# Kernel tuning notes

Hardware: AMD Instinct MI355X
Metric: run time of the kernel (lower is better)

Reference implementation:

```python
import jax, jax.numpy as jnp
import numpy as np

# Segment geometry (from init_kwargs): modes ['u','uv','v'] -> out_v = alpha * x_u @ W_uv
U = 128
V = 128
IN_OFF = [0, 128, 256, 384]
W_OFF = [k * U * V for k in range(8)]          # [0,16384,...,114688]
OUT_OFF = [0, 128, 256, 384]
IN_STRIDE = 512
OUT_STRIDE = 512
W_STRIDE = 8 * U * V                           # 131072
# (in_seg, w_seg, out_seg, coefficient)
PATHS = [(0, 0, 0, 1.0), (1, 1, 1, 1.0), (2, 2, 2, 1.0), (3, 3, 3, 1.0),
         (0, 4, 1, 0.5), (1, 5, 2, 0.5), (2, 6, 3, 0.5), (3, 7, 0, 0.5)]
B = 32768
E = 4  # num_embeddings (experts)


def setup_inputs() -> dict:
    key = jax.random.key(0)
    k1, k2, k3 = jax.random.split(key, 3)
    tensor_in = jax.random.normal(k1, (B, IN_STRIDE), dtype=jnp.float32)
    tensor_w = jax.random.normal(k2, (E, W_STRIDE), dtype=jnp.float32)
    tensor_w_id = jax.random.randint(k3, (B,), 0, E, dtype=jnp.int32)
    return {"tensor_in": tensor_in, "tensor_w": tensor_w, "tensor_w_id": tensor_w_id}


def _batch_linear(tensor_in, tensor_w, tensor_w_id):
    """Segmented path-indexed grouped linear (cuEquivariance BatchLinear fwd).

    tensor_in: [B, IN_STRIDE]; tensor_w: [E, W_STRIDE]; tensor_w_id: [B] int in [0,E).
    For each path (i, j, k, alpha):
        out[b, OUT_OFF[k]:+V] += alpha * x[b, IN_OFF[i]:+U] @ W[w_id[b], seg j].reshape(U, V)
    """
    nb = tensor_in.shape[0]
    ne = tensor_w.shape[0]
    onehot = jax.nn.one_hot(tensor_w_id, ne, dtype=tensor_in.dtype)  # [B, E]
    out = jnp.zeros((nb, OUT_STRIDE), dtype=tensor_in.dtype)
    for (i, j, k, a) in PATHS:
        x = tensor_in[:, IN_OFF[i]:IN_OFF[i] + U]                    # [B, U]
        w_seg = tensor_w[:, W_OFF[j]:W_OFF[j] + U * V].reshape(ne, U, V)
        # masked per-expert dense GEMMs (small fixed expert count)
        y = jnp.zeros((nb, V), dtype=tensor_in.dtype)
        for e in range(ne):
            y = y + onehot[:, e:e + 1] * (x @ w_seg[e])              # [B, V]
        out = out.at[:, OUT_OFF[k]:OUT_OFF[k] + V].add(a * y)
    return out


def reference(tensor_in, tensor_w, tensor_w_id):
    return _batch_linear(tensor_in, tensor_w, tensor_w_id)
```

## Files before the change

### kernel.cpp

```cpp
#include <hip/hip_runtime.h>
#include <stdint.h>

#define U 128
#define V 128
#define IN_STRIDE 512
#define OUT_STRIDE 512
#define W_STRIDE (8 * U * V)
#define NB 32768
#define NE 4

#define WS_WSHUF 0
#define WS_CNT   1048576
#define WS_SORT  1048640

typedef __bf16 bf16x8 __attribute__((ext_vector_type(8)));
typedef float f32x16 __attribute__((ext_vector_type(16)));
typedef unsigned int u32x4 __attribute__((ext_vector_type(4)));
typedef unsigned int u32x2 __attribute__((ext_vector_type(2)));

static __device__ __forceinline__ unsigned short f2bf(float f) {
    unsigned int u = __builtin_bit_cast(unsigned int, f);
    u += 0x7FFFu + ((u >> 16) & 1u);
    return (unsigned short)(u >> 16);
}

__global__ void prep_kernel(const float* __restrict__ w, unsigned short* __restrict__ wshuf,
                            unsigned int* __restrict__ cnt) {
    if (blockIdx.x == 0 && threadIdx.x < NE) cnt[threadIdx.x] = 0u;
    int t = blockIdx.x * 256 + threadIdx.x;
    int lane = t & 63;
    int kt = (t >> 6) & 7;
    int nt = (t >> 9) & 3;
    int s  = (t >> 11) & 7;
    int e  = (t >> 14) & 3;
    int kbase = kt * 16 + ((lane >> 5) << 3);
    int n = nt * 32 + (lane & 31);
    const float* src = w + (size_t)e * W_STRIDE + (size_t)s * (U * V) + n;
    float sc = (s >= 4) ? 0.5f : 1.0f;
    __attribute__((aligned(16))) unsigned short o[8];
#pragma unroll
    for (int j = 0; j < 8; j++) o[j] = f2bf(src[(size_t)(kbase + j) * V] * sc);
    *(u32x4*)(wshuf + (size_t)t * 8) = *(const u32x4*)o;
}

__global__ void scatter_kernel(const int* __restrict__ wid, unsigned int* __restrict__ cnt,
                               int* __restrict__ sorted) {
    __shared__ unsigned int lcnt[NE];
    __shared__ unsigned int lbase[NE];
    int t = threadIdx.x;
    if (t < NE) lcnt[t] = 0u;
    __syncthreads();
    int i = blockIdx.x * 256 + t;
    int e = wid[i];
    unsigned int lpos = atomicAdd(&lcnt[e], 1u);
    __syncthreads();
    if (t < NE) lbase[t] = atomicAdd(&cnt[t], lcnt[t]);
    __syncthreads();
    sorted[e * NB + (int)(lbase[e] + lpos)] = i;
}

__global__ __launch_bounds__(512, 4) void gemm_kernel(
        const float* __restrict__ x, const unsigned short* __restrict__ wshuf,
        const unsigned int* __restrict__ cnt, const int* __restrict__ sorted,
        float* __restrict__ out) {
    const int rowbase = blockIdx.x * 64;
    __shared__ unsigned short lds[64 * 512];
    __shared__ int rowid[64];

    const unsigned int p1 = cnt[0];
    const unsigned int p2 = p1 + cnt[1];
    const unsigned int p3 = p2 + cnt[2];

    const int t = threadIdx.x;

    {
        int r = t >> 3;
        int g = t & 7;
        unsigned int l = (unsigned int)(rowbase + r);
        int e = (l >= p1) + (l >= p2) + (l >= p3);
        unsigned int pe = (e == 0) ? 0u : (e == 1) ? p1 : (e == 2) ? p2 : p3;
        int row = sorted[e * NB + (int)(l - pe)];
        if (g == 0) rowid[r] = row;
        const float* xr = x + (size_t)row * IN_STRIDE;
        unsigned short* Lrow = lds + r * 512;
        int rs = r & 7;
#pragma unroll
        for (int i = 0; i < 16; i++) {
            int c = g * 4 + i * 32;
            float4 v = *(const float4*)(xr + c);
            __attribute__((aligned(8))) unsigned short h[4];
            h[0] = f2bf(v.x); h[1] = f2bf(v.y); h[2] = f2bf(v.z); h[3] = f2bf(v.w);
            int off = ((((c >> 3) ^ rs)) << 3) + (c & 7);
            *(u32x2*)(Lrow + off) = *(const u32x2*)h;
        }
    }

    const int w = t >> 6, lane = t & 63;
    const int kout = w >> 1, nhalf = w & 1;
    const int m0 = lane & 31;
    const int khalf3 = (lane >> 5);
    const int rowswz = m0 & 7;

    const unsigned int l0 = (unsigned int)(rowbase + m0);
    const unsigned int l1 = l0 + 32u;
    const int e0 = (l0 >= p1) + (l0 >= p2) + (l0 >= p3);
    const int e1 = (l1 >= p1) + (l1 >= p2) + (l1 >= p3);
    const unsigned int lh = (unsigned int)rowbase, lt = (unsigned int)(rowbase + 63);
    const int ehead = (lh >= p1) + (lh >= p2) + (lh >= p3);
    const int etail = (lt >= p1) + (lt >= p2) + (lt >= p3);

    __syncthreads();

    f32x16 acc00 = {}, acc01 = {}, acc10 = {}, acc11 = {};

    const int xbs1 = (kout + 3) & 3;
    int xbs[2] = {kout, xbs1};
    int sgs[2] = {kout, xbs1 + 4};

    const unsigned short* Lr0 = lds + m0 * 512;
    const unsigned short* Lr1 = lds + (m0 + 32) * 512;

    if (ehead == etail) {
        const int eu = ehead;
#pragma unroll
        for (int c = 0; c < 2; c++) {
            int colbase3 = xbs[c] * 16;
            const unsigned short* wseg =
                wshuf + ((size_t)((eu * 8 + sgs[c]) * 4 + nhalf * 2) * 8) * 512 + (size_t)lane * 8;
#pragma unroll
            for (int kt = 0; kt < 8; kt++) {
                int kabs3 = colbase3 + kt * 2 + khalf3;
                int packoff = ((kabs3 ^ rowswz) << 3);
                bf16x8 a0 = __builtin_bit_cast(bf16x8, *(const u32x4*)(Lr0 + packoff));
                bf16x8 a1 = __builtin_bit_cast(bf16x8, *(const u32x4*)(Lr1 + packoff));
                bf16x8 b0 = __builtin_bit_cast(bf16x8, *(const u32x4*)(wseg + (size_t)kt * 512));
                bf16x8 b1 = __builtin_bit_cast(bf16x8, *(const u32x4*)(wseg + (size_t)(8 + kt) * 512));
                acc00 = __builtin_amdgcn_mfma_f32_32x32x16_bf16(a0, b0, acc00, 0, 0, 0);
                acc01 = __builtin_amdgcn_mfma_f32_32x32x16_bf16(a0, b1, acc01, 0, 0, 0);
                acc10 = __builtin_amdgcn_mfma_f32_32x32x16_bf16(a1, b0, acc10, 0, 0, 0);
                acc11 = __builtin_amdgcn_mfma_f32_32x32x16_bf16(a1, b1, acc11, 0, 0, 0);
            }
        }
    } else {
        unsigned int msk0[4], msk1[4];
#pragma unroll
        for (int e = 0; e < 4; e++) {
            msk0[e] = (e0 == e) ? 0xFFFFFFFFu : 0u;
            msk1[e] = (e1 == e) ? 0xFFFFFFFFu : 0u;
        }
#pragma unroll
        for (int c = 0; c < 2; c++) {
            int colbase3 = xbs[c] * 16;
#pragma unroll
            for (int kt = 0; kt < 8; kt++) {
                int kabs3 = colbase3 + kt * 2 + khalf3;
                int packoff = ((kabs3 ^ rowswz) << 3);
                u32x4 a0u = *(const u32x4*)(Lr0 + packoff);
                u32x4 a1u = *(const u32x4*)(Lr1 + packoff);
#pragma unroll
                for (int e = 0; e < 4; e++) {
                    const unsigned short* wseg =
                        wshuf + ((size_t)((e * 8 + sgs[c]) * 4 + nhalf * 2) * 8) * 512;
                    bf16x8 b0 = __builtin_bit_cast(bf16x8, *(const u32x4*)(wseg + (size_t)kt * 512 + lane * 8));
                    bf16x8 b1 = __builtin_bit_cast(bf16x8, *(const u32x4*)(wseg + (size_t)(8 + kt) * 512 + lane * 8));
                    u32x4 mm0 = {msk0[e], msk0[e], msk0[e], msk0[e]};
                    u32x4 mm1 = {msk1[e], msk1[e], msk1[e], msk1[e]};
                    bf16x8 a0m = __builtin_bit_cast(bf16x8, a0u & mm0);
                    bf16x8 a1m = __builtin_bit_cast(bf16x8, a1u & mm1);
                    acc00 = __builtin_amdgcn_mfma_f32_32x32x16_bf16(a0m, b0, acc00, 0, 0, 0);
                    acc01 = __builtin_amdgcn_mfma_f32_32x32x16_bf16(a0m, b1, acc01, 0, 0, 0);
                    acc10 = __builtin_amdgcn_mfma_f32_32x32x16_bf16(a1m, b0, acc10, 0, 0, 0);
                    acc11 = __builtin_amdgcn_mfma_f32_32x32x16_bf16(a1m, b1, acc11, 0, 0, 0);
                }
            }
        }
    }

    const int colb = kout * 128 + nhalf * 64 + m0;
    const int rh = (lane >> 5) << 2;
#pragma unroll
    for (int q = 0; q < 4; q++) {
#pragma unroll
        for (int d = 0; d < 4; d++) {
            int reg = q * 4 + d;
            int rl = d + 8 * q + rh;
            float* o0 = out + (size_t)rowid[rl] * OUT_STRIDE + colb;
            float* o1 = out + (size_t)rowid[rl + 32] * OUT_STRIDE + colb;
            o0[0]  = acc00[reg];
            o0[32] = acc01[reg];
            o1[0]  = acc10[reg];
            o1[32] = acc11[reg];
        }
    }
}

extern "C" void kernel_launch(void* const* d_in, const int* in_sizes, int n_in,
                              void* d_out, int out_size, void* d_ws, size_t ws_size,
                              hipStream_t stream) {
    const float* x = (const float*)d_in[0];
    const float* w = (const float*)d_in[1];
    const int* wid = (const int*)d_in[2];
    float* out = (float*)d_out;

    unsigned short* wshuf = (unsigned short*)((char*)d_ws + WS_WSHUF);
    unsigned int* cnt = (unsigned int*)((char*)d_ws + WS_CNT);
    int* sorted = (int*)((char*)d_ws + WS_SORT);

    prep_kernel<<<256, 256, 0, stream>>>(w, wshuf, cnt);
    scatter_kernel<<<128, 256, 0, stream>>>(wid, cnt, sorted);
    gemm_kernel<<<512, 512, 0, stream>>>(x, wshuf, cnt, sorted, out);
}
```

Before: 134.9 us.

## Drop LDS staging; load activations directly into MFMA registers with 32-row tiles

The GEMM kernel no longer stages bf16-converted activation rows in shared memory. Each wave now loads its A fragment straight from global fp32, converts it in registers, and covers all four 32-column N tiles of one output block, with 32 rows per workgroup of 256 threads. This removes the LDS footprint, the barrier and the staging pass, and should raise occupancy. In exchange each x element is loaded and converted by two waves instead of once, weight fragments are reused across fewer rows, and the output row ids are recomputed from the sorted index rather than read from shared memory.

```diff
diff --git a/kernel.cpp b/kernel.cpp
--- a/kernel.cpp
+++ b/kernel.cpp
@@ -16,7 +16,6 @@
 typedef __bf16 bf16x8 __attribute__((ext_vector_type(8)));
 typedef float f32x16 __attribute__((ext_vector_type(16)));
 typedef unsigned int u32x4 __attribute__((ext_vector_type(4)));
-typedef unsigned int u32x2 __attribute__((ext_vector_type(2)));
 
 static __device__ __forceinline__ unsigned short f2bf(float f) {
     unsigned int u = __builtin_bit_cast(unsigned int, f);
@@ -59,137 +58,111 @@
     sorted[e * NB + (int)(lbase[e] + lpos)] = i;
 }
 
-__global__ __launch_bounds__(512, 4) void gemm_kernel(
+__global__ __launch_bounds__(256, 4) void gemm_kernel(
         const float* __restrict__ x, const unsigned short* __restrict__ wshuf,
         const unsigned int* __restrict__ cnt, const int* __restrict__ sorted,
         float* __restrict__ out) {
-    const int rowbase = blockIdx.x * 64;
-    __shared__ unsigned short lds[64 * 512];
-    __shared__ int rowid[64];
-
+    const int rowbase = blockIdx.x * 32;
     const unsigned int p1 = cnt[0];
     const unsigned int p2 = p1 + cnt[1];
     const unsigned int p3 = p2 + cnt[2];
 
     const int t = threadIdx.x;
-
-    {
-        int r = t >> 3;
-        int g = t & 7;
-        unsigned int l = (unsigned int)(rowbase + r);
-        int e = (l >= p1) + (l >= p2) + (l >= p3);
-        unsigned int pe = (e == 0) ? 0u : (e == 1) ? p1 : (e == 2) ? p2 : p3;
-        int row = sorted[e * NB + (int)(l - pe)];
-        if (g == 0) rowid[r] = row;
-        const float* xr = x + (size_t)row * IN_STRIDE;
-        unsigned short* Lrow = lds + r * 512;
-        int rs = r & 7;
-#pragma unroll
-        for (int i = 0; i < 16; i++) {
-            int c = g * 4 + i * 32;
-            float4 v = *(const float4*)(xr + c);
-            __attribute__((aligned(8))) unsigned short h[4];
-            h[0] = f2bf(v.x); h[1] = f2bf(v.y); h[2] = f2bf(v.z); h[3] = f2bf(v.w);
-            int off = ((((c >> 3) ^ rs)) << 3) + (c & 7);
-            *(u32x2*)(Lrow + off) = *(const u32x2*)h;
-        }
-    }
-
-    const int w = t >> 6, lane = t & 63;
-    const int kout = w >> 1, nhalf = w & 1;
+    const int kout = t >> 6;
+    const int lane = t & 63;
     const int m0 = lane & 31;
-    const int khalf3 = (lane >> 5);
-    const int rowswz = m0 & 7;
+    const int khalf = lane >> 5;
 
     const unsigned int l0 = (unsigned int)(rowbase + m0);
-    const unsigned int l1 = l0 + 32u;
     const int e0 = (l0 >= p1) + (l0 >= p2) + (l0 >= p3);
-    const int e1 = (l1 >= p1) + (l1 >= p2) + (l1 >= p3);
-    const unsigned int lh = (unsigned int)rowbase, lt = (unsigned int)(rowbase + 63);
+    const unsigned int pe0 = (e0 == 0) ? 0u : (e0 == 1) ? p1 : (e0 == 2) ? p2 : p3;
+    const int arow = sorted[e0 * NB + (int)(l0 - pe0)];
+    const float* xr = x + (size_t)arow * IN_STRIDE + khalf * 8;
+
+    const unsigned int lh = (unsigned int)rowbase, lt = (unsigned int)(rowbase + 31);
     const int ehead = (lh >= p1) + (lh >= p2) + (lh >= p3);
     const int etail = (lt >= p1) + (lt >= p2) + (lt >= p3);
-
-    __syncthreads();
-
-    f32x16 acc00 = {}, acc01 = {}, acc10 = {}, acc11 = {};
 
     const int xbs1 = (kout + 3) & 3;
     int xbs[2] = {kout, xbs1};
     int sgs[2] = {kout, xbs1 + 4};
 
-    const unsigned short* Lr0 = lds + m0 * 512;
-    const unsigned short* Lr1 = lds + (m0 + 32) * 512;
+    f32x16 acc[4] = {};
 
     if (ehead == etail) {
         const int eu = ehead;
 #pragma unroll
         for (int c = 0; c < 2; c++) {
-            int colbase3 = xbs[c] * 16;
-            const unsigned short* wseg =
-                wshuf + ((size_t)((eu * 8 + sgs[c]) * 4 + nhalf * 2) * 8) * 512 + (size_t)lane * 8;
+            const unsigned short* wb =
+                wshuf + (size_t)((eu * 8 + sgs[c]) * 4) * 4096 + (size_t)lane * 8;
+            const float* xc = xr + xbs[c] * 128;
 #pragma unroll
             for (int kt = 0; kt < 8; kt++) {
-                int kabs3 = colbase3 + kt * 2 + khalf3;
-                int packoff = ((kabs3 ^ rowswz) << 3);
-                bf16x8 a0 = __builtin_bit_cast(bf16x8, *(const u32x4*)(Lr0 + packoff));
-                bf16x8 a1 = __builtin_bit_cast(bf16x8, *(const u32x4*)(Lr1 + packoff));
-                bf16x8 b0 = __builtin_bit_cast(bf16x8, *(const u32x4*)(wseg + (size_t)kt * 512));
-                bf16x8 b1 = __builtin_bit_cast(bf16x8, *(const u32x4*)(wseg + (size_t)(8 + kt) * 512));
-                acc00 = __builtin_amdgcn_mfma_f32_32x32x16_bf16(a0, b0, acc00, 0, 0, 0);
-                acc01 = __builtin_amdgcn_mfma_f32_32x32x16_bf16(a0, b1, acc01, 0, 0, 0);
-                acc10 = __builtin_amdgcn_mfma_f32_32x32x16_bf16(a1, b0, acc10, 0, 0, 0);
-                acc11 = __builtin_amdgcn_mfma_f32_32x32x16_bf16(a1, b1, acc11, 0, 0, 0);
+                float4 va = *(const float4*)(xc + kt * 16);
+                float4 vb = *(const float4*)(xc + kt * 16 + 4);
+                bf16x8 a;
+                a[0] = (__bf16)va.x; a[1] = (__bf16)va.y;
+                a[2] = (__bf16)va.z; a[3] = (__bf16)va.w;
+                a[4] = (__bf16)vb.x; a[5] = (__bf16)vb.y;
+                a[6] = (__bf16)vb.z; a[7] = (__bf16)vb.w;
+#pragma unroll
+                for (int nt = 0; nt < 4; nt++) {
+                    bf16x8 b = __builtin_bit_cast(bf16x8,
+                        *(const u32x4*)(wb + (size_t)(nt * 8 + kt) * 512));
+                    acc[nt] = __builtin_amdgcn_mfma_f32_32x32x16_bf16(a, b, acc[nt], 0, 0, 0);
+                }
             }
         }
     } else {
-        unsigned int msk0[4], msk1[4];
+        unsigned int msk[4];
 #pragma unroll
-        for (int e = 0; e < 4; e++) {
-            msk0[e] = (e0 == e) ? 0xFFFFFFFFu : 0u;
-            msk1[e] = (e1 == e) ? 0xFFFFFFFFu : 0u;
-        }
+        for (int e = 0; e < 4; e++) msk[e] = (e0 == e) ? 0xFFFFFFFFu : 0u;
 #pragma unroll
         for (int c = 0; c < 2; c++) {
-            int colbase3 = xbs[c] * 16;
+            const float* xc = xr + xbs[c] * 128;
 #pragma unroll
             for (int kt = 0; kt < 8; kt++) {
-                int kabs3 = colbase3 + kt * 2 + khalf3;
-                int packoff = ((kabs3 ^ rowswz) << 3);
-                u32x4 a0u = *(const u32x4*)(Lr0 + packoff);
-                u32x4 a1u = *(const u32x4*)(Lr1 + packoff);
+                float4 va = *(const float4*)(xc + kt * 16);
+                float4 vb = *(const float4*)(xc + kt * 16 + 4);
+                __attribute__((aligned(16))) unsigned short au[8];
+                au[0] = f2bf(va.x); au[1] = f2bf(va.y);
+                au[2] = f2bf(va.z); au[3] = f2bf(va.w);
+                au[4] = f2bf(vb.x); au[5] = f2bf(vb.y);
+                au[6] = f2bf(vb.z); au[7] = f2bf(vb.w);
+                u32x4 araw = *(const u32x4*)au;
 #pragma unroll
                 for (int e = 0; e < 4; e++) {
-                    const unsigned short* wseg =
-                        wshuf + ((size_t)((e * 8 + sgs[c]) * 4 + nhalf * 2) * 8) * 512;
-                    bf16x8 b0 = __builtin_bit_cast(bf16x8, *(const u32x4*)(wseg + (size_t)kt * 512 + lane * 8));
-                    bf16x8 b1 = __builtin_bit_cast(bf16x8, *(const u32x4*)(wseg + (size_t)(8 + kt) * 512 + lane * 8));
-                    u32x4 mm0 = {msk0[e], msk0[e], msk0[e], msk0[e]};
-                    u32x4 mm1 = {msk1[e], msk1[e], msk1[e], msk1[e]};
-                    bf16x8 a0m = __builtin_bit_cast(bf16x8, a0u & mm0);
-                    bf16x8 a1m = __builtin_bit_cast(bf16x8, a1u & mm1);
-                    acc00 = __builtin_amdgcn_mfma_f32_32x32x16_bf16(a0m, b0, acc00, 0, 0, 0);
-                    acc01 = __builtin_amdgcn_mfma_f32_32x32x16_bf16(a0m, b1, acc01, 0, 0, 0);
-                    acc10 = __builtin_amdgcn_mfma_f32_32x32x16_bf16(a1m, b0, acc10, 0, 0, 0);
-                    acc11 = __builtin_amdgcn_mfma_f32_32x32x16_bf16(a1m, b1, acc11, 0, 0, 0);
+                    u32x4 mm = {msk[e], msk[e], msk[e], msk[e]};
+                    bf16x8 am = __builtin_bit_cast(bf16x8, araw & mm);
+                    const unsigned short* wb =
+                        wshuf + (size_t)((e * 8 + sgs[c]) * 4) * 4096 + (size_t)lane * 8;
+#pragma unroll
+                    for (int nt = 0; nt < 4; nt++) {
+                        bf16x8 b = __builtin_bit_cast(bf16x8,
+                            *(const u32x4*)(wb + (size_t)(nt * 8 + kt) * 512));
+                        acc[nt] = __builtin_amdgcn_mfma_f32_32x32x16_bf16(am, b, acc[nt], 0, 0, 0);
+                    }
                 }
             }
         }
     }
 
-    const int colb = kout * 128 + nhalf * 64 + m0;
-    const int rh = (lane >> 5) << 2;
+    const int colb = kout * 128 + m0;
+    const int rh = khalf << 2;
 #pragma unroll
     for (int q = 0; q < 4; q++) {
 #pragma unroll
         for (int d = 0; d < 4; d++) {
             int reg = q * 4 + d;
-            int rl = d + 8 * q + rh;
-            float* o0 = out + (size_t)rowid[rl] * OUT_STRIDE + colb;
-            float* o1 = out + (size_t)rowid[rl + 32] * OUT_STRIDE + colb;
-            o0[0]  = acc00[reg];
-            o0[32] = acc01[reg];
-            o1[0]  = acc10[reg];
-            o1[32] = acc11[reg];
+            unsigned int ls = (unsigned int)(rowbase + d + 8 * q + rh);
+            int es = (ls >= p1) + (ls >= p2) + (ls >= p3);
+            unsigned int pes = (es == 0) ? 0u : (es == 1) ? p1 : (es == 2) ? p2 : p3;
+            int orow = sorted[es * NB + (int)(ls - pes)];
+            float* o = out + (size_t)orow * OUT_STRIDE + colb;
+            o[0]  = acc[0][reg];
+            o[32] = acc[1][reg];
+            o[64] = acc[2][reg];
+            o[96] = acc[3][reg];
         }
     }
 }
@@ -208,5 +181,5 @@
 
     prep_kernel<<<256, 256, 0, stream>>>(w, wshuf, cnt);
     scatter_kernel<<<128, 256, 0, stream>>>(wid, cnt, sorted);
-    gemm_kernel<<<512, 512, 0, stream>>>(x, wshuf, cnt, sorted, out);
+    gemm_kernel<<<1024, 256, 0, stream>>>(x, wshuf, cnt, sorted, out);
 }
```

After: 200.5 us. +48.6%, slower.
